# Kernel tuning notes

Measured on AMD Instinct MI355X. Metric: run time of the kernel, lower is better.

## Reference

```python
import jax, jax.numpy as jnp
import numpy as np

N_KNOTS = 4
OUT_DIM = 512
IN_DIM = 512
BATCH = 4096


def setup_inputs() -> dict:
    key = jax.random.key(0)
    k1, k2, k3 = jax.random.split(key, 3)
    # inputs: [B, IN_DIM + N_KNOTS]; last N_KNOTS cols are phase blend weights
    x = jax.random.normal(k1, (BATCH, IN_DIM + N_KNOTS), dtype=jnp.float32)
    # make the phase columns a valid convex-ish blend (softmax), as in PFNN usage
    phase = jax.nn.softmax(x[:, -N_KNOTS:], axis=-1)
    x = jnp.concatenate([x[:, :-N_KNOTS], phase], axis=-1)
    bound = np.sqrt(6.0 / (OUT_DIM * IN_DIM))
    weight_knots = jax.random.uniform(k2, (N_KNOTS, OUT_DIM, IN_DIM), dtype=jnp.float32,
                                      minval=-bound, maxval=bound)
    bias_knots = jnp.zeros((N_KNOTS, OUT_DIM), dtype=jnp.float32)
    return {"inputs": x, "weight_knots": weight_knots, "bias_knots": bias_knots}


def reference(inputs, weight_knots, bias_knots):
    # Split features and phase blend coefficients
    p = inputs[:, -N_KNOTS:]          # [B, K]
    feat = inputs[:, :-N_KNOTS]       # [B, IN]
    # Original: wi = sum_k p[:,k] * W[k]  ([B,out,in]); res = wi @ feat + bi.
    # Fused equivalent: contract W with feat first, then blend over knots,
    # avoiding the [B,out,in] intermediate.
    # knot_out: [B, K, OUT]
    knot_out = jnp.einsum('koi,bi->bko', weight_knots, feat)
    res = jnp.einsum('bk,bko->bo', p, knot_out) + p @ bias_knots  # [B, OUT]
    res = jax.nn.elu(res)
    return res
```

## Files before the change

### kernel.cpp

```cpp
#include <hip/hip_runtime.h>

#define BATCH 4096
#define IN_DIM 512
#define OUT_DIM 512
#define NK 4
#define SX (IN_DIM + NK)
#define BM 64
#define BN 64
#define BK 64

typedef short bf16x8 __attribute__((ext_vector_type(8)));
typedef float f32x4 __attribute__((ext_vector_type(4)));

__device__ __forceinline__ unsigned short f2bf(float f) {
    unsigned int u = __float_as_uint(f);
    u = u + 0x7FFFu + ((u >> 16) & 1u);
    return (unsigned short)(u >> 16);
}

__device__ __forceinline__ void gload_lds16(const void* g, void* l) {
    __builtin_amdgcn_global_load_lds(
        (const __attribute__((address_space(1))) void*)g,
        (__attribute__((address_space(3))) void*)l, 16, 0, 0);
}

__global__ __launch_bounds__(256) void convert_kernel(
    const float* __restrict__ x, const float* __restrict__ w,
    unsigned short* __restrict__ wb, unsigned short* __restrict__ fb)
{
    const int WCH = NK * OUT_DIM * IN_DIM / 4;
    int g = blockIdx.x * 256 + threadIdx.x;
    if (g < WCH) {
        const float4 v = reinterpret_cast<const float4*>(w)[g];
        unsigned short h[4] = {f2bf(v.x), f2bf(v.y), f2bf(v.z), f2bf(v.w)};
        *reinterpret_cast<uint2*>(&wb[g * 4]) = *reinterpret_cast<const uint2*>(h);
    } else {
        int idx = g - WCH;
        int row = idx >> 7;
        int c   = (idx & 127) * 4;
        const float4 v = *reinterpret_cast<const float4*>(&x[(size_t)row * SX + c]);
        unsigned short h[4] = {f2bf(v.x), f2bf(v.y), f2bf(v.z), f2bf(v.w)};
        *reinterpret_cast<uint2*>(&fb[row * IN_DIM + c]) = *reinterpret_cast<const uint2*>(h);
    }
}

__global__ __launch_bounds__(256) void mpl_gemm(
    const unsigned short* __restrict__ fb,
    const unsigned short* __restrict__ wb,
    const float* __restrict__ x,
    const float* __restrict__ bias,
    float* __restrict__ out)
{
    __shared__ unsigned short As[BM * BK];
    __shared__ unsigned short Bs[NK * BN * BK];

    const int tid  = threadIdx.x;
    const int lane = tid & 63;
    const int wid  = tid >> 6;
    const int wr   = (wid >> 1) * 32;
    const int wc   = (wid & 1) * 32;
    const int R0   = blockIdx.x * BM;
    const int C0   = blockIdx.y * BN;

    f32x4 acc[NK][2][2] = {};
    const int cl = lane & 15;
    const int kb = (lane >> 4) * 8;

    for (int kt = 0; kt < IN_DIM / BK; ++kt) {
        const int k0 = kt * BK;
        __syncthreads();
        #pragma unroll
        for (int j = 0; j < 2; ++j) {
            int ch  = j * 256 + wid * 64 + lane;
            int row = ch >> 3;
            int c   = ch & 7;
            const unsigned short* src =
                fb + (size_t)(R0 + row) * IN_DIM + k0 + ((c ^ (row & 7)) << 3);
            gload_lds16(src, &As[ch * 8]);
        }
        #pragma unroll
        for (int j = 0; j < 8; ++j) {
            int ch  = j * 256 + wid * 64 + lane;
            int kn  = ch >> 9;
            int rem = ch & 511;
            int row = rem >> 3;
            int c   = rem & 7;
            const unsigned short* src =
                wb + (size_t)kn * OUT_DIM * IN_DIM + (size_t)(C0 + row) * IN_DIM
                   + k0 + ((c ^ (row & 7)) << 3);
            gload_lds16(src, &Bs[ch * 8]);
        }
        __syncthreads();
        #pragma unroll
        for (int kk = 0; kk < BK; kk += 32) {
            bf16x8 af[2];
            #pragma unroll
            for (int m = 0; m < 2; ++m) {
                int row  = wr + m * 16 + cl;
                int boff = (row * 128 + (kk + kb) * 2) ^ ((row & 7) << 4);
                af[m] = *reinterpret_cast<const bf16x8*>(
                    reinterpret_cast<const char*>(As) + boff);
            }
            #pragma unroll
            for (int kn = 0; kn < NK; ++kn) {
                bf16x8 bfr[2];
                #pragma unroll
                for (int n = 0; n < 2; ++n) {
                    int row  = wc + n * 16 + cl;
                    int boff = (row * 128 + (kk + kb) * 2) ^ ((row & 7) << 4);
                    bfr[n] = *reinterpret_cast<const bf16x8*>(
                        reinterpret_cast<const char*>(Bs) + kn * 8192 + boff);
                }
                #pragma unroll
                for (int m = 0; m < 2; ++m)
                    #pragma unroll
                    for (int n = 0; n < 2; ++n)
                        acc[kn][m][n] = __builtin_amdgcn_mfma_f32_16x16x32_bf16(
                            af[m], bfr[n], acc[kn][m][n], 0, 0, 0);
            }
        }
    }

    const int rl = (lane >> 4) * 4;
    float bcol[2][NK];
    #pragma unroll
    for (int n = 0; n < 2; ++n)
        #pragma unroll
        for (int k = 0; k < NK; ++k)
            bcol[n][k] = bias[k * OUT_DIM + C0 + wc + n * 16 + cl];

    #pragma unroll
    for (int m = 0; m < 2; ++m) {
        #pragma unroll
        for (int r = 0; r < 4; ++r) {
            const int row = R0 + wr + m * 16 + rl + r;
            const float4 p = *reinterpret_cast<const float4*>(&x[(size_t)row * SX + IN_DIM]);
            const float pk[4] = {p.x, p.y, p.z, p.w};
            #pragma unroll
            for (int n = 0; n < 2; ++n) {
                float v = 0.f;
                #pragma unroll
                for (int k = 0; k < NK; ++k)
                    v += pk[k] * (acc[k][m][n][r] + bcol[n][k]);
                v = (v > 0.f) ? v : expm1f(v);
                out[(size_t)row * OUT_DIM + C0 + wc + n * 16 + cl] = v;
            }
        }
    }
}

#define LDT 72
__global__ __launch_bounds__(256) void mpl_kernel_fb(
    const float* __restrict__ x, const float* __restrict__ w,
    const float* __restrict__ bias, float* __restrict__ out)
{
    __shared__ unsigned short As[BM][LDT];
    __shared__ unsigned short Bs[NK][BN][LDT];
    const int tid = threadIdx.x, lane = tid & 63, wid = tid >> 6;
    const int wr = (wid >> 1) * 32, wc = (wid & 1) * 32;
    const int R0 = blockIdx.x * BM, C0 = blockIdx.y * BN;
    f32x4 acc[NK][2][2] = {};
    const int cl = lane & 15, kb = (lane >> 4) * 8;
    for (int kt = 0; kt < IN_DIM / BK; ++kt) {
        const int k0 = kt * BK;
        __syncthreads();
        #pragma unroll
        for (int j = 0; j < 4; ++j) {
            int f = tid + 256 * j, row = f >> 4, c4 = (f & 15) * 4;
            const float4 v = *reinterpret_cast<const float4*>(&x[(size_t)(R0 + row) * SX + k0 + c4]);
            unsigned short h[4] = {f2bf(v.x), f2bf(v.y), f2bf(v.z), f2bf(v.w)};
            *reinterpret_cast<uint2*>(&As[row][c4]) = *reinterpret_cast<const uint2*>(h);
        }
        #pragma unroll
        for (int kn = 0; kn < NK; ++kn)
            #pragma unroll
            for (int j = 0; j < 4; ++j) {
                int f = tid + 256 * j, row = f >> 4, c4 = (f & 15) * 4;
                const float4 v = *reinterpret_cast<const float4*>(
                    &w[(size_t)kn * OUT_DIM * IN_DIM + (size_t)(C0 + row) * IN_DIM + k0 + c4]);
                unsigned short h[4] = {f2bf(v.x), f2bf(v.y), f2bf(v.z), f2bf(v.w)};
                *reinterpret_cast<uint2*>(&Bs[kn][row][c4]) = *reinterpret_cast<const uint2*>(h);
            }
        __syncthreads();
        #pragma unroll
        for (int kk = 0; kk < BK; kk += 32) {
            bf16x8 af[2];
            #pragma unroll
            for (int m = 0; m < 2; ++m)
                af[m] = *reinterpret_cast<const bf16x8*>(&As[wr + m * 16 + cl][kk + kb]);
            #pragma unroll
            for (int kn = 0; kn < NK; ++kn) {
                bf16x8 bfr[2];
                #pragma unroll
                for (int n = 0; n < 2; ++n)
                    bfr[n] = *reinterpret_cast<const bf16x8*>(&Bs[kn][wc + n * 16 + cl][kk + kb]);
                #pragma unroll
                for (int m = 0; m < 2; ++m)
                    #pragma unroll
                    for (int n = 0; n < 2; ++n)
                        acc[kn][m][n] = __builtin_amdgcn_mfma_f32_16x16x32_bf16(
                            af[m], bfr[n], acc[kn][m][n], 0, 0, 0);
            }
        }
    }
    const int rl = (lane >> 4) * 4;
    float bcol[2][NK];
    #pragma unroll
    for (int n = 0; n < 2; ++n)
        #pragma unroll
        for (int k = 0; k < NK; ++k)
            bcol[n][k] = bias[k * OUT_DIM + C0 + wc + n * 16 + cl];
    #pragma unroll
    for (int m = 0; m < 2; ++m)
        #pragma unroll
        for (int r = 0; r < 4; ++r) {
            const int row = R0 + wr + m * 16 + rl + r;
            const float4 p = *reinterpret_cast<const float4*>(&x[(size_t)row * SX + IN_DIM]);
            const float pk[4] = {p.x, p.y, p.z, p.w};
            #pragma unroll
            for (int n = 0; n < 2; ++n) {
                float v = 0.f;
                #pragma unroll
                for (int k = 0; k < NK; ++k)
                    v += pk[k] * (acc[k][m][n][r] + bcol[n][k]);
                v = (v > 0.f) ? v : expm1f(v);
                out[(size_t)row * OUT_DIM + C0 + wc + n * 16 + cl] = v;
            }
        }
}

extern "C" void kernel_launch(void* const* d_in, const int* in_sizes, int n_in,
                              void* d_out, int out_size, void* d_ws, size_t ws_size,
                              hipStream_t stream) {
    const float* x    = (const float*)d_in[0];
    const float* w    = (const float*)d_in[1];
    const float* bias = (const float*)d_in[2];
    float* out        = (float*)d_out;

    const size_t wb_bytes = (size_t)NK * OUT_DIM * IN_DIM * 2;
    const size_t fb_bytes = (size_t)BATCH * IN_DIM * 2;

    if (ws_size < wb_bytes + fb_bytes) {
        dim3 grid(BATCH / BM, OUT_DIM / BN);
        mpl_kernel_fb<<<grid, dim3(256), 0, stream>>>(x, w, bias, out);
        return;
    }

    unsigned short* wb = (unsigned short*)d_ws;
    unsigned short* fb = (unsigned short*)((char*)d_ws + wb_bytes);

    const int total_chunks = NK * OUT_DIM * IN_DIM / 4 + BATCH * IN_DIM / 4;
    convert_kernel<<<dim3(total_chunks / 256), dim3(256), 0, stream>>>(x, w, wb, fb);

    dim3 grid(BATCH / BM, OUT_DIM / BN);
    mpl_gemm<<<grid, dim3(256), 0, stream>>>(fb, wb, x, bias, out);
}
```

Measured before the change: 26.92 us.

## Double-buffer LDS tiles in bf16 GEMM to overlap global loads with MFMA

The main GEMM kernel now holds two LDS buffers for the A and B tiles. It issues the async global-to-LDS loads for the next K step before computing on the current buffer, so each iteration needs one barrier instead of two. The aim is to hide global memory latency behind MFMA work. LDS use doubles to about 80 KB per block, which may lower occupancy. Correctness relies on the compiler's wait handling for the async LDS loads before the barrier.

```diff
diff --git a/kernel.cpp b/kernel.cpp
--- a/kernel.cpp
+++ b/kernel.cpp
@@ -51,8 +51,8 @@
     const float* __restrict__ bias,
     float* __restrict__ out)
 {
-    __shared__ unsigned short As[BM * BK];
-    __shared__ unsigned short Bs[NK * BN * BK];
+    __shared__ unsigned short As[2 * BM * BK];
+    __shared__ unsigned short Bs[2 * NK * BN * BK];
 
     const int tid  = threadIdx.x;
     const int lane = tid & 63;
@@ -66,31 +66,31 @@
     const int cl = lane & 15;
     const int kb = (lane >> 4) * 8;
 
-    for (int kt = 0; kt < IN_DIM / BK; ++kt) {
-        const int k0 = kt * BK;
-        __syncthreads();
+    auto stage = [&](int b, int k0) {
         #pragma unroll
         for (int j = 0; j < 2; ++j) {
-            int ch  = j * 256 + wid * 64 + lane;
+            int ch  = j * 256 + tid;
             int row = ch >> 3;
             int c   = ch & 7;
-            const unsigned short* src =
-                fb + (size_t)(R0 + row) * IN_DIM + k0 + ((c ^ (row & 7)) << 3);
-            gload_lds16(src, &As[ch * 8]);
+            gload_lds16(fb + (size_t)(R0 + row) * IN_DIM + k0 + ((c ^ (row & 7)) << 3),
+                        &As[b * BM * BK + ch * 8]);
         }
         #pragma unroll
         for (int j = 0; j < 8; ++j) {
-            int ch  = j * 256 + wid * 64 + lane;
+            int ch  = j * 256 + tid;
             int kn  = ch >> 9;
             int rem = ch & 511;
             int row = rem >> 3;
             int c   = rem & 7;
-            const unsigned short* src =
-                wb + (size_t)kn * OUT_DIM * IN_DIM + (size_t)(C0 + row) * IN_DIM
-                   + k0 + ((c ^ (row & 7)) << 3);
-            gload_lds16(src, &Bs[ch * 8]);
-        }
-        __syncthreads();
+            gload_lds16(wb + (size_t)kn * OUT_DIM * IN_DIM + (size_t)(C0 + row) * IN_DIM
+                           + k0 + ((c ^ (row & 7)) << 3),
+                        &Bs[b * NK * BN * BK + ch * 8]);
+        }
+    };
+
+    auto compute = [&](int b) {
+        const char* Ab = reinterpret_cast<const char*>(As) + b * BM * BK * 2;
+        const char* Bb = reinterpret_cast<const char*>(Bs) + b * NK * BN * BK * 2;
         #pragma unroll
         for (int kk = 0; kk < BK; kk += 32) {
             bf16x8 af[2];
@@ -98,8 +98,7 @@
             for (int m = 0; m < 2; ++m) {
                 int row  = wr + m * 16 + cl;
                 int boff = (row * 128 + (kk + kb) * 2) ^ ((row & 7) << 4);
-                af[m] = *reinterpret_cast<const bf16x8*>(
-                    reinterpret_cast<const char*>(As) + boff);
+                af[m] = *reinterpret_cast<const bf16x8*>(Ab + boff);
             }
             #pragma unroll
             for (int kn = 0; kn < NK; ++kn) {
@@ -108,8 +107,7 @@
                 for (int n = 0; n < 2; ++n) {
                     int row  = wc + n * 16 + cl;
                     int boff = (row * 128 + (kk + kb) * 2) ^ ((row & 7) << 4);
-                    bfr[n] = *reinterpret_cast<const bf16x8*>(
-                        reinterpret_cast<const char*>(Bs) + kn * 8192 + boff);
+                    bfr[n] = *reinterpret_cast<const bf16x8*>(Bb + kn * 8192 + boff);
                 }
                 #pragma unroll
                 for (int m = 0; m < 2; ++m)
@@ -119,6 +117,15 @@
                             af[m], bfr[n], acc[kn][m][n], 0, 0, 0);
             }
         }
+    };
+
+    stage(0, 0);
+    __syncthreads();
+    for (int kt = 0; kt < IN_DIM / BK; ++kt) {
+        const int cur = kt & 1;
+        if (kt < IN_DIM / BK - 1) stage(cur ^ 1, (kt + 1) * BK);
+        compute(cur);
+        if (kt < IN_DIM / BK - 1) __syncthreads();
     }
 
     const int rl = (lane >> 4) * 4;
@@ -154,8 +161,8 @@
     const float* __restrict__ x, const float* __restrict__ w,
     const float* __restrict__ bias, float* __restrict__ out)
 {
-    __shared__ unsigned short As[BM][LDT];
-    __shared__ unsigned short Bs[NK][BN][LDT];
+    __shared__ unsigned short Asf[BM][LDT];
+    __shared__ unsigned short Bsf[NK][BN][LDT];
     const int tid = threadIdx.x, lane = tid & 63, wid = tid >> 6;
     const int wr = (wid >> 1) * 32, wc = (wid & 1) * 32;
     const int R0 = blockIdx.x * BM, C0 = blockIdx.y * BN;
@@ -169,7 +176,7 @@
             int f = tid + 256 * j, row = f >> 4, c4 = (f & 15) * 4;
             const float4 v = *reinterpret_cast<const float4*>(&x[(size_t)(R0 + row) * SX + k0 + c4]);
             unsigned short h[4] = {f2bf(v.x), f2bf(v.y), f2bf(v.z), f2bf(v.w)};
-            *reinterpret_cast<uint2*>(&As[row][c4]) = *reinterpret_cast<const uint2*>(h);
+            *reinterpret_cast<uint2*>(&Asf[row][c4]) = *reinterpret_cast<const uint2*>(h);
         }
         #pragma unroll
         for (int kn = 0; kn < NK; ++kn)
@@ -179,7 +186,7 @@
                 const float4 v = *reinterpret_cast<const float4*>(
                     &w[(size_t)kn * OUT_DIM * IN_DIM + (size_t)(C0 + row) * IN_DIM + k0 + c4]);
                 unsigned short h[4] = {f2bf(v.x), f2bf(v.y), f2bf(v.z), f2bf(v.w)};
-                *reinterpret_cast<uint2*>(&Bs[kn][row][c4]) = *reinterpret_cast<const uint2*>(h);
+                *reinterpret_cast<uint2*>(&Bsf[kn][row][c4]) = *reinterpret_cast<const uint2*>(h);
             }
         __syncthreads();
         #pragma unroll
@@ -187,13 +194,13 @@
             bf16x8 af[2];
             #pragma unroll
             for (int m = 0; m < 2; ++m)
-                af[m] = *reinterpret_cast<const bf16x8*>(&As[wr + m * 16 + cl][kk + kb]);
+                af[m] = *reinterpret_cast<const bf16x8*>(&Asf[wr + m * 16 + cl][kk + kb]);
             #pragma unroll
             for (int kn = 0; kn < NK; ++kn) {
                 bf16x8 bfr[2];
                 #pragma unroll
                 for (int n = 0; n < 2; ++n)
-                    bfr[n] = *reinterpret_cast<const bf16x8*>(&Bs[kn][wc + n * 16 + cl][kk + kb]);
+                    bfr[n] = *reinterpret_cast<const bf16x8*>(&Bsf[kn][wc + n * 16 + cl][kk + kb]);
                 #pragma unroll
                 for (int m = 0; m < 2; ++m)
                     #pragma unroll
```

Result: no change. 27.04 us (+0.5%).
